# Optimization experiments

Hardware: AMD Instinct MI355X
Metric: run time of the kernel (lower is better)

## Reference

```python
import jax, jax.numpy as jnp
import numpy as np

GROUP_SIZE = 256
QMIN_W, QMAX_W = -8, 7  # int4
QMIN_A, QMAX_A = -128, 127  # int8


def per_token_fake_quant(x):
    """torchao choose_qparams_per_token_asymmetric + quant + dequant (int8)."""
    mn = jnp.minimum(jnp.min(x, axis=-1, keepdims=True), 0.0)
    mx = jnp.maximum(jnp.max(x, axis=-1, keepdims=True), 0.0)
    eps = jnp.finfo(jnp.float32).eps
    scale = jnp.maximum((mx - mn) / float(QMAX_A - QMIN_A), eps)
    dmin = mn / scale
    dmax = mx / scale
    zp = jnp.where((QMIN_A + dmin) + (QMAX_A + dmax) > 0, QMIN_A - dmin, QMAX_A - dmax)
    zp = jnp.round(jnp.clip(zp, QMIN_A, QMAX_A))
    q = jnp.clip(jnp.round(x / scale) + zp, QMIN_A, QMAX_A)
    return (q - zp) * scale


def setup_inputs() -> dict:
    key = jax.random.key(0)
    k1, k2, k3, k4 = jax.random.split(key, 4)
    T, O, I = 8192, 4096, 4096
    x = jax.random.normal(k1, (T, I), dtype=jnp.float32)
    weight = jax.random.randint(k2, (O, I), QMIN_W, QMAX_W + 1, dtype=jnp.int32)
    scales = jax.random.uniform(k3, (O, I // GROUP_SIZE), dtype=jnp.float32,
                                minval=0.005, maxval=0.02)
    zeros = jnp.round(jax.random.uniform(k4, (O, I // GROUP_SIZE), dtype=jnp.float32,
                                         minval=-4.0, maxval=4.0))
    return {"x": x, "weight": weight, "scales": scales, "zeros": zeros}


def reference(x, weight, scales, zeros):
    # dynamic per-token int8 fake-quant of the activation
    x_dq = per_token_fake_quant(x.astype(jnp.float32))
    # groupwise int4 weight dequant: (w - zero) * scale per group
    O, I = weight.shape
    w = weight.astype(jnp.float32).reshape(O, I // GROUP_SIZE, GROUP_SIZE)
    w_dq = ((w - zeros[..., None]) * scales[..., None]).reshape(O, I)
    # linear: [T, I] @ [I, O] -> [T, O]
    return jnp.einsum('ti,oi->to', x_dq, w_dq)
```

## Files before the change

### kernel.cpp

```cpp
#include <hip/hip_runtime.h>
#include <hip/hip_bf16.h>
#include <math.h>

typedef __attribute__((ext_vector_type(8))) __bf16 bf16x8;
typedef __attribute__((ext_vector_type(4))) float f32x4;

#define BM 128
#define BN 128
#define BK 64

__device__ __forceinline__ void glds16(const void* g, void* l) {
  __builtin_amdgcn_global_load_lds(
      (const __attribute__((address_space(1))) void*)g,
      (__attribute__((address_space(3))) void*)l, 16, 0, 0);
}

__device__ __forceinline__ unsigned short f2bf(float f) {
  __hip_bfloat16 h = __float2bfloat16(f);
  return __builtin_bit_cast(unsigned short, h);
}

__global__ void prep_fused(const float* __restrict__ x,
                           ushort* __restrict__ xq, int T,
                           const int* __restrict__ w,
                           const float* __restrict__ scales,
                           const float* __restrict__ zeros,
                           ushort* __restrict__ wq, int I, int G) {
  const int tid = threadIdx.x;
  if (blockIdx.x < (unsigned)T) {
    const int row = blockIdx.x;
    const float4* xr = (const float4*)(x + (size_t)row * I);
    float4 v[4];
    float mn = 0.f, mx = 0.f;
#pragma unroll
    for (int i = 0; i < 4; ++i) {
      v[i] = xr[tid + i * 256];
      mn = fminf(mn, fminf(fminf(v[i].x, v[i].y), fminf(v[i].z, v[i].w)));
      mx = fmaxf(mx, fmaxf(fmaxf(v[i].x, v[i].y), fmaxf(v[i].z, v[i].w)));
    }
#pragma unroll
    for (int off = 32; off > 0; off >>= 1) {
      mn = fminf(mn, __shfl_down(mn, off));
      mx = fmaxf(mx, __shfl_down(mx, off));
    }
    __shared__ float smn[4], smx[4], sp[3];
    const int wave = tid >> 6, lane = tid & 63;
    if (lane == 0) { smn[wave] = mn; smx[wave] = mx; }
    __syncthreads();
    if (tid == 0) {
      mn = fminf(fminf(smn[0], smn[1]), fminf(smn[2], smn[3]));
      mx = fmaxf(fmaxf(smx[0], smx[1]), fmaxf(smx[2], smx[3]));
      float scale = fmaxf((mx - mn) / 255.0f, 1.1920928955078125e-07f);
      float dmin = mn / scale, dmax = mx / scale;
      float zp = ((-128.0f + dmin) + (127.0f + dmax) > 0.0f)
                     ? (-128.0f - dmin)
                     : (127.0f - dmax);
      zp = rintf(fminf(fmaxf(zp, -128.0f), 127.0f));
      sp[0] = scale;
      sp[1] = zp;
      sp[2] = 1.0f / scale;
    }
    __syncthreads();
    const float scale = sp[0], zp = sp[1], rs = sp[2];
    ushort4* xo = (ushort4*)(xq + (size_t)row * I);
#pragma unroll
    for (int i = 0; i < 4; ++i) {
      ushort4 o;
      float q;
      q = fminf(fmaxf(rintf(v[i].x * rs) + zp, -128.f), 127.f);
      o.x = f2bf((q - zp) * scale);
      q = fminf(fmaxf(rintf(v[i].y * rs) + zp, -128.f), 127.f);
      o.y = f2bf((q - zp) * scale);
      q = fminf(fmaxf(rintf(v[i].z * rs) + zp, -128.f), 127.f);
      o.z = f2bf((q - zp) * scale);
      q = fminf(fmaxf(rintf(v[i].w * rs) + zp, -128.f), 127.f);
      o.w = f2bf((q - zp) * scale);
      xo[tid + i * 256] = o;
    }
  } else {
    const int o = blockIdx.x - T;
    const int4* wr = (const int4*)(w + (size_t)o * I);
    ushort4* wo = (ushort4*)(wq + (size_t)o * I);
#pragma unroll
    for (int it = 0; it < 4; ++it) {
      const int chunk = it * 256 + tid;
      const int g = chunk >> 6;
      const float s = scales[(size_t)o * G + g];
      const float z = zeros[(size_t)o * G + g];
      const int4 wv = wr[chunk];
      ushort4 ov;
      ov.x = f2bf(((float)wv.x - z) * s);
      ov.y = f2bf(((float)wv.y - z) * s);
      ov.z = f2bf(((float)wv.z - z) * s);
      ov.w = f2bf(((float)wv.w - z) * s);
      wo[chunk] = ov;
    }
  }
}

__global__ __launch_bounds__(256) void gemm_bt(const ushort* __restrict__ A,
                                               const ushort* __restrict__ B,
                                               float* __restrict__ C, int M,
                                               int N, int K) {
  __shared__ __align__(16) ushort As[BM * BK];
  __shared__ __align__(16) ushort Bs[BN * BK];
  const int tid = threadIdx.x;
  const int wave = tid >> 6, lane = tid & 63;
  const int wm = (wave >> 1) * 64, wn = (wave & 1) * 64;
  const int bm0 = blockIdx.y * BM, bn0 = blockIdx.x * BN;

  const int ldr = lane >> 3;
  const int ldk = ((lane & 7) ^ ldr) * 8;
  const ushort* Ag = A + (size_t)(bm0 + wave * 32 + ldr) * K + ldk;
  const ushort* Bg = B + (size_t)(bn0 + wave * 32 + ldr) * K + ldk;
  ushort* Asw = &As[(wave * 32) * BK];
  ushort* Bsw = &Bs[(wave * 32) * BK];

  f32x4 acc[4][4];
#pragma unroll
  for (int i = 0; i < 4; ++i)
#pragma unroll
    for (int j = 0; j < 4; ++j) acc[i][j] = (f32x4){0.f, 0.f, 0.f, 0.f};

  const int mrow = lane & 15;
  const int kc = lane >> 4;
  const int sw = mrow & 7;

  for (int k0 = 0; k0 < K; k0 += BK) {
#pragma unroll
    for (int it = 0; it < 4; ++it) {
      glds16(Ag + (size_t)(it * 8) * K + k0, Asw + (it * 8) * BK);
      glds16(Bg + (size_t)(it * 8) * K + k0, Bsw + (it * 8) * BK);
    }
    __syncthreads();
#pragma unroll
    for (int ks = 0; ks < 2; ++ks) {
      const int chunk = ((ks * 4 + kc) ^ sw) * 8;
      bf16x8 af[4], bfv[4];
#pragma unroll
      for (int i = 0; i < 4; ++i) {
        af[i] = *(const bf16x8*)&As[(wm + i * 16 + mrow) * BK + chunk];
        bfv[i] = *(const bf16x8*)&Bs[(wn + i * 16 + mrow) * BK + chunk];
      }
#pragma unroll
      for (int i = 0; i < 4; ++i)
#pragma unroll
        for (int j = 0; j < 4; ++j)
          acc[i][j] = __builtin_amdgcn_mfma_f32_16x16x32_bf16(
              af[i], bfv[j], acc[i][j], 0, 0, 0);
    }
    __syncthreads();
  }

  const int col = lane & 15;
  const int rq = (lane >> 4) * 4;
#pragma unroll
  for (int i = 0; i < 4; ++i)
#pragma unroll
    for (int j = 0; j < 4; ++j) {
      const int r0 = bm0 + wm + i * 16 + rq;
      const int c = bn0 + wn + j * 16 + col;
#pragma unroll
      for (int r = 0; r < 4; ++r)
        C[(size_t)(r0 + r) * N + c] = acc[i][j][r];
    }
}

extern "C" void kernel_launch(void* const* d_in, const int* in_sizes, int n_in,
                              void* d_out, int out_size, void* d_ws,
                              size_t ws_size, hipStream_t stream) {
  const float* x = (const float*)d_in[0];
  const int* w = (const int*)d_in[1];
  const float* scales = (const float*)d_in[2];
  const float* zeros = (const float*)d_in[3];
  float* out = (float*)d_out;

  const double ii =
      sqrt((double)in_sizes[0] * (double)in_sizes[1] / (double)out_size);
  const int I = (int)(ii + 0.5);
  const int T = in_sizes[0] / I;
  const int O = in_sizes[1] / I;
  const int G = I / 256;

  ushort* xq = (ushort*)d_ws;
  ushort* wq = xq + (size_t)T * I;

  prep_fused<<<T + O, 256, 0, stream>>>(x, xq, T, w, scales, zeros, wq, I, G);
  gemm_bt<<<dim3(O / BN, T / BM), 256, 0, stream>>>(xq, wq, out, T, O, I);
}
```

Measured before the change: 591.9 us.

## Rewrite GEMM as 256x256 double-buffered 8-wave kernel with staged prefetch

Replaces the 128x128 single-buffered GEMM with a 256x256-tile kernel using 512 threads, double-buffered LDS, and interleaved quarter-phase loads and MFMA blocks separated by barriers and priority raises. Adds an XCD-aware block-index swizzle for L2 locality. The aim is to overlap global-to-LDS loads with matrix math and raise arithmetic intensity per tile. In exchange it needs 128KB of LDS and many more accumulator registers, which may limit occupancy, and the manual vmcnt waits have to stay correct.

```diff
diff --git a/kernel.cpp b/kernel.cpp
--- a/kernel.cpp
+++ b/kernel.cpp
@@ -5,8 +5,8 @@
 typedef __attribute__((ext_vector_type(8))) __bf16 bf16x8;
 typedef __attribute__((ext_vector_type(4))) float f32x4;
 
-#define BM 128
-#define BN 128
+#define BM 256
+#define BN 256
 #define BK 64
 
 __device__ __forceinline__ void glds16(const void* g, void* l) {
@@ -98,72 +98,180 @@
   }
 }
 
-__global__ __launch_bounds__(256) void gemm_bt(const ushort* __restrict__ A,
-                                               const ushort* __restrict__ B,
-                                               float* __restrict__ C, int M,
-                                               int N, int K) {
-  __shared__ __align__(16) ushort As[BM * BK];
-  __shared__ __align__(16) ushort Bs[BN * BK];
+__global__ __launch_bounds__(512, 2) void gemm_bt256(
+    const ushort* __restrict__ A, const ushort* __restrict__ B,
+    float* __restrict__ C, int M, int N, int K) {
+  __shared__ __align__(16) ushort As[2][BM * BK];
+  __shared__ __align__(16) ushort Bs[2][BN * BK];
   const int tid = threadIdx.x;
   const int wave = tid >> 6, lane = tid & 63;
-  const int wm = (wave >> 1) * 64, wn = (wave & 1) * 64;
-  const int bm0 = blockIdx.y * BM, bn0 = blockIdx.x * BN;
+  const int wm = wave >> 2;
+  const int wn = wave & 3;
+
+  const int nwg = gridDim.x;
+  const int bid = blockIdx.x;
+  const int swz =
+      ((nwg & 7) == 0) ? ((bid & 7) * (nwg >> 3) + (bid >> 3)) : bid;
+  const int ntn = N / BN;
+  const int by = swz / ntn, bx = swz % ntn;
+  const int bm0 = by * BM, bn0 = bx * BN;
 
   const int ldr = lane >> 3;
-  const int ldk = ((lane & 7) ^ ldr) * 8;
-  const ushort* Ag = A + (size_t)(bm0 + wave * 32 + ldr) * K + ldk;
-  const ushort* Bg = B + (size_t)(bn0 + wave * 32 + ldr) * K + ldk;
-  ushort* Asw = &As[(wave * 32) * BK];
-  ushort* Bsw = &Bs[(wave * 32) * BK];
-
-  f32x4 acc[4][4];
-#pragma unroll
-  for (int i = 0; i < 4; ++i)
-#pragma unroll
-    for (int j = 0; j < 4; ++j) acc[i][j] = (f32x4){0.f, 0.f, 0.f, 0.f};
+  const int ldc = ((lane & 7) ^ ldr) * 8;
+  const ushort* Ag = A + (size_t)(bm0 + wave * 16 + ldr) * K + ldc;
+  const ushort* Bg = B + (size_t)(bn0 + wave * 16 + ldr) * K + ldc;
+
+#define STAGE_A(b, h, kt)                                          \
+  do {                                                             \
+    glds16(Ag + (size_t)((h) * 128) * K + (size_t)(kt) * BK,       \
+           &As[b][((h) * 128 + wave * 16) * BK]);                  \
+    glds16(Ag + (size_t)((h) * 128 + 8) * K + (size_t)(kt) * BK,   \
+           &As[b][((h) * 128 + wave * 16 + 8) * BK]);              \
+  } while (0)
+#define STAGE_B(b, h, kt)                                          \
+  do {                                                             \
+    glds16(Bg + (size_t)((h) * 128) * K + (size_t)(kt) * BK,       \
+           &Bs[b][((h) * 128 + wave * 16) * BK]);                  \
+    glds16(Bg + (size_t)((h) * 128 + 8) * K + (size_t)(kt) * BK,   \
+           &Bs[b][((h) * 128 + wave * 16 + 8) * BK]);              \
+  } while (0)
 
   const int mrow = lane & 15;
   const int kc = lane >> 4;
   const int sw = mrow & 7;
-
-  for (int k0 = 0; k0 < K; k0 += BK) {
-#pragma unroll
-    for (int it = 0; it < 4; ++it) {
-      glds16(Ag + (size_t)(it * 8) * K + k0, Asw + (it * 8) * BK);
-      glds16(Bg + (size_t)(it * 8) * K + k0, Bsw + (it * 8) * BK);
-    }
-    __syncthreads();
-#pragma unroll
-    for (int ks = 0; ks < 2; ++ks) {
-      const int chunk = ((ks * 4 + kc) ^ sw) * 8;
-      bf16x8 af[4], bfv[4];
-#pragma unroll
-      for (int i = 0; i < 4; ++i) {
-        af[i] = *(const bf16x8*)&As[(wm + i * 16 + mrow) * BK + chunk];
-        bfv[i] = *(const bf16x8*)&Bs[(wn + i * 16 + mrow) * BK + chunk];
-      }
-#pragma unroll
-      for (int i = 0; i < 4; ++i)
-#pragma unroll
-        for (int j = 0; j < 4; ++j)
-          acc[i][j] = __builtin_amdgcn_mfma_f32_16x16x32_bf16(
-              af[i], bfv[j], acc[i][j], 0, 0, 0);
-    }
-    __syncthreads();
+  const int c0 = (kc ^ sw) * 8;
+  const int c1 = ((4 + kc) ^ sw) * 8;
+  const int aBase = (wm * 128 + mrow) * BK;
+  const int bBase = (wn * 64 + mrow) * BK;
+
+  f32x4 acc[8][4];
+#pragma unroll
+  for (int i = 0; i < 8; ++i)
+#pragma unroll
+    for (int j = 0; j < 4; ++j) acc[i][j] = (f32x4){0.f, 0.f, 0.f, 0.f};
+
+  const int NT = K / BK;
+
+  STAGE_A(0, 0, 0);
+  STAGE_A(0, 1, 0);
+  STAGE_B(0, 0, 0);
+  STAGE_B(0, 1, 0);
+  STAGE_B(1, 0, 1);
+  STAGE_B(1, 1, 1);
+  __builtin_amdgcn_sched_barrier(0);
+  asm volatile("s_waitcnt vmcnt(4)" ::: "memory");
+  __builtin_amdgcn_s_barrier();
+
+  bf16x8 a[4][2], b[4][2];
+
+  for (int kt = 0; kt < NT; ++kt) {
+    const int cur = kt & 1, nxt = cur ^ 1;
+    const ushort* Ac = As[cur];
+    const ushort* Bc = Bs[cur];
+
+#pragma unroll
+    for (int mi = 0; mi < 4; ++mi) {
+      a[mi][0] = *(const bf16x8*)&Ac[aBase + mi * (16 * BK) + c0];
+      a[mi][1] = *(const bf16x8*)&Ac[aBase + mi * (16 * BK) + c1];
+    }
+#pragma unroll
+    for (int ni = 0; ni < 2; ++ni) {
+      b[ni][0] = *(const bf16x8*)&Bc[bBase + ni * (16 * BK) + c0];
+      b[ni][1] = *(const bf16x8*)&Bc[bBase + ni * (16 * BK) + c1];
+    }
+    if (kt + 1 < NT) STAGE_A(nxt, 0, kt + 1);
+    __builtin_amdgcn_sched_barrier(0);
+    __builtin_amdgcn_s_barrier();
+    __builtin_amdgcn_s_setprio(1);
+#pragma unroll
+    for (int ks = 0; ks < 2; ++ks)
+#pragma unroll
+      for (int mi = 0; mi < 4; ++mi)
+#pragma unroll
+        for (int ni = 0; ni < 2; ++ni)
+          acc[mi][ni] = __builtin_amdgcn_mfma_f32_16x16x32_bf16(
+              a[mi][ks], b[ni][ks], acc[mi][ni], 0, 0, 0);
+    __builtin_amdgcn_s_setprio(0);
+    __builtin_amdgcn_sched_barrier(0);
+    __builtin_amdgcn_s_barrier();
+
+#pragma unroll
+    for (int ni = 2; ni < 4; ++ni) {
+      b[ni][0] = *(const bf16x8*)&Bc[bBase + ni * (16 * BK) + c0];
+      b[ni][1] = *(const bf16x8*)&Bc[bBase + ni * (16 * BK) + c1];
+    }
+    if (kt + 1 < NT) STAGE_A(nxt, 1, kt + 1);
+    __builtin_amdgcn_sched_barrier(0);
+    __builtin_amdgcn_s_barrier();
+    __builtin_amdgcn_s_setprio(1);
+#pragma unroll
+    for (int ks = 0; ks < 2; ++ks)
+#pragma unroll
+      for (int mi = 0; mi < 4; ++mi)
+#pragma unroll
+        for (int ni = 2; ni < 4; ++ni)
+          acc[mi][ni] = __builtin_amdgcn_mfma_f32_16x16x32_bf16(
+              a[mi][ks], b[ni][ks], acc[mi][ni], 0, 0, 0);
+    __builtin_amdgcn_s_setprio(0);
+    __builtin_amdgcn_sched_barrier(0);
+    __builtin_amdgcn_s_barrier();
+
+#pragma unroll
+    for (int mi = 0; mi < 4; ++mi) {
+      a[mi][0] = *(const bf16x8*)&Ac[aBase + (mi + 4) * (16 * BK) + c0];
+      a[mi][1] = *(const bf16x8*)&Ac[aBase + (mi + 4) * (16 * BK) + c1];
+    }
+    if (kt + 2 < NT) STAGE_B(cur, 0, kt + 2);
+    __builtin_amdgcn_sched_barrier(0);
+    __builtin_amdgcn_s_barrier();
+    __builtin_amdgcn_s_setprio(1);
+#pragma unroll
+    for (int ks = 0; ks < 2; ++ks)
+#pragma unroll
+      for (int mi = 0; mi < 4; ++mi)
+#pragma unroll
+        for (int ni = 2; ni < 4; ++ni)
+          acc[mi + 4][ni] = __builtin_amdgcn_mfma_f32_16x16x32_bf16(
+              a[mi][ks], b[ni][ks], acc[mi + 4][ni], 0, 0, 0);
+    __builtin_amdgcn_s_setprio(0);
+    __builtin_amdgcn_sched_barrier(0);
+    __builtin_amdgcn_s_barrier();
+
+    if (kt + 2 < NT) STAGE_B(cur, 1, kt + 2);
+    __builtin_amdgcn_sched_barrier(0);
+    if (kt < NT - 2)
+      asm volatile("s_waitcnt vmcnt(4)" ::: "memory");
+    else
+      asm volatile("s_waitcnt vmcnt(0)" ::: "memory");
+    __builtin_amdgcn_s_barrier();
+    __builtin_amdgcn_s_setprio(1);
+#pragma unroll
+    for (int ks = 0; ks < 2; ++ks)
+#pragma unroll
+      for (int mi = 0; mi < 4; ++mi)
+#pragma unroll
+        for (int ni = 0; ni < 2; ++ni)
+          acc[mi + 4][ni] = __builtin_amdgcn_mfma_f32_16x16x32_bf16(
+              a[mi][ks], b[ni][ks], acc[mi + 4][ni], 0, 0, 0);
+    __builtin_amdgcn_s_setprio(0);
+    __builtin_amdgcn_sched_barrier(0);
+    __builtin_amdgcn_s_barrier();
   }
 
   const int col = lane & 15;
   const int rq = (lane >> 4) * 4;
 #pragma unroll
-  for (int i = 0; i < 4; ++i)
-#pragma unroll
-    for (int j = 0; j < 4; ++j) {
-      const int r0 = bm0 + wm + i * 16 + rq;
-      const int c = bn0 + wn + j * 16 + col;
+  for (int mi = 0; mi < 8; ++mi)
+#pragma unroll
+    for (int ni = 0; ni < 4; ++ni) {
+      const int r0 = bm0 + wm * 128 + mi * 16 + rq;
+      const int c = bn0 + wn * 64 + ni * 16 + col;
 #pragma unroll
       for (int r = 0; r < 4; ++r)
-        C[(size_t)(r0 + r) * N + c] = acc[i][j][r];
-    }
+        C[(size_t)(r0 + r) * N + c] = acc[mi][ni][r];
+    }
+#undef STAGE_A
+#undef STAGE_B
 }
 
 extern "C" void kernel_launch(void* const* d_in, const int* in_sizes, int n_in,
@@ -186,5 +294,5 @@
   ushort* wq = xq + (size_t)T * I;
 
   prep_fused<<<T + O, 256, 0, stream>>>(x, xq, T, w, scales, zeros, wq, I, G);
-  gemm_bt<<<dim3(O / BN, T / BM), 256, 0, stream>>>(xq, wq, out, T, O, I);
-}
+  gemm_bt256<<<(O / BN) * (T / BM), 512, 0, stream>>>(xq, wq, out, T, O, I);
+}
```

Result: faster. 529.9 us (-10.5%).
